# Performance work log

Measured on AMD Instinct MI355X. Metric: run time of the kernel, lower is better.

Reference implementation:

```python
import jax, jax.numpy as jnp
import numpy as np

R, TR = 47, 2  # response_size, treat_size


def _lstm_cell(x, h, c, Wih, Whh, bih, bhh):
    # PyTorch gate order: i, f, g, o
    gates = x @ Wih.T + h @ Whh.T + bih + bhh
    i, f, g, o = jnp.split(gates, 4, axis=-1)
    c_new = jax.nn.sigmoid(f) * c + jax.nn.sigmoid(i) * jnp.tanh(g)
    h_new = jax.nn.sigmoid(o) * jnp.tanh(c_new)
    return h_new, c_new


def setup_inputs() -> dict:
    key = jax.random.key(0)
    B, T = 256, 2048
    ks = jax.random.split(key, 20)

    def u(k, shape, H):
        s = 1.0 / np.sqrt(H).astype(np.float32)
        return jax.random.uniform(k, shape, jnp.float32, -s, s)

    return {
        "x_r": jax.random.normal(ks[0], (B, T, R), jnp.float32),
        "x_t": jax.random.normal(ks[1], (B, T, TR), jnp.float32),
        # r_rnn: 2-layer LSTM, input 49 -> hidden 47
        "r_Wih0": u(ks[2], (4 * R, R + TR), R), "r_Whh0": u(ks[3], (4 * R, R), R),
        "r_bih0": u(ks[4], (4 * R,), R), "r_bhh0": u(ks[5], (4 * R,), R),
        "r_Wih1": u(ks[6], (4 * R, R), R), "r_Whh1": u(ks[7], (4 * R, R), R),
        "r_bih1": u(ks[8], (4 * R,), R), "r_bhh1": u(ks[9], (4 * R,), R),
        # t_rnn: 2-layer LSTM, input 96 -> hidden 2
        "t_Wih0": u(ks[10], (4 * TR, 2 * R + TR), TR), "t_Whh0": u(ks[11], (4 * TR, TR), TR),
        "t_bih0": u(ks[12], (4 * TR,), TR), "t_bhh0": u(ks[13], (4 * TR,), TR),
        "t_Wih1": u(ks[14], (4 * TR, TR), TR), "t_Whh1": u(ks[15], (4 * TR, TR), TR),
        "t_bih1": u(ks[16], (4 * TR,), TR), "t_bhh1": u(ks[17], (4 * TR,), TR),
    }


def reference(x_r, x_t,
              r_Wih0, r_Whh0, r_bih0, r_bhh0, r_Wih1, r_Whh1, r_bih1, r_bhh1,
              t_Wih0, t_Whh0, t_bih0, t_bhh0, t_Wih1, t_Whh1, t_bih1, t_bhh1):
    B = x_r.shape[0]
    zR = jnp.zeros((B, R), x_r.dtype)
    zT = jnp.zeros((B, TR), x_r.dtype)

    def step(carry, xs):
        hr0, cr0, hr1, cr1, ht0, ct0, ht1, ct1 = carry
        r, t = xs  # [B,47], [B,2]
        r_in = jnp.concatenate([r, t], axis=-1)              # [B,49]
        hr0, cr0 = _lstm_cell(r_in, hr0, cr0, r_Wih0, r_Whh0, r_bih0, r_bhh0)
        hr1, cr1 = _lstm_cell(hr0, hr1, cr1, r_Wih1, r_Whh1, r_bih1, r_bhh1)
        t_in = jnp.concatenate([r_in, hr1], axis=-1)         # [B,96]
        ht0, ct0 = _lstm_cell(t_in, ht0, ct0, t_Wih0, t_Whh0, t_bih0, t_bhh0)
        ht1, ct1 = _lstm_cell(ht0, ht1, ct1, t_Wih1, t_Whh1, t_bih1, t_bhh1)
        return (hr0, cr0, hr1, cr1, ht0, ct0, ht1, ct1), (hr1, ht1)

    init = (zR, zR, zR, zR, zT, zT, zT, zT)
    xs = (x_r.transpose(1, 0, 2), x_t.transpose(1, 0, 2))    # time-major
    _, (r_seq, t_seq) = jax.lax.scan(step, init, xs)         # [T,B,47], [T,B,2]
    return (r_seq.transpose(1, 0, 2), t_seq.transpose(1, 0, 2))
```

## Files before the change

### kernel.cpp

```cpp
#include <hip/hip_runtime.h>

#define T_STEPS 2048
#define TOTAL   2080

typedef float f2 __attribute__((ext_vector_type(2)));
typedef _Float16 h2 __attribute__((ext_vector_type(2)));

__device__ __forceinline__ float fast_rcp(float x) { return __builtin_amdgcn_rcpf(x); }

__device__ __forceinline__ float sig_f(float x) {
    return fast_rcp(1.0f + __expf(-x));
}
__device__ __forceinline__ float tanh_f(float x) {
    float e = __expf(-2.0f * x);
    return fmaf(2.0f, fast_rcp(1.0f + e), -1.0f);
}
__device__ __forceinline__ float gate_act(float x, float zm, float sm, float sa) {
    float e = __expf(-x * zm);
    return fmaf(fast_rcp(1.0f + e), sm, sa);
}

#if __has_builtin(__builtin_amdgcn_fdot2)
#define FDOT2(a, b, c) __builtin_amdgcn_fdot2((a), (b), (c), false)
#else
__device__ __forceinline__ float FDOT2(h2 a, h2 b, float c) {
    return fmaf((float)a.x, (float)b.x, fmaf((float)a.y, (float)b.y, c));
}
#endif

#define LDS_BARRIER() asm volatile("s_waitcnt lgkmcnt(0)\n\ts_barrier" ::: "memory")

#define DPP_BCAST0 0x00
#define DPP_BCAST1 0x55
#define DPP_BCAST2 0xAA
#define DPP_BCAST3 0xFF
#define DPP_PAIR   0xF5
#define DPP_ROR4   0x124
#define DPP_ROR8   0x128
template<int CTRL>
__device__ __forceinline__ float dppf(float x) {
    int r = __builtin_amdgcn_update_dpp(0, __builtin_bit_cast(int, x), CTRL, 0xF, 0xF, true);
    return __builtin_bit_cast(float, r);
}

__device__ __forceinline__ void loadx4(float (&dst)[4], const float* __restrict__ x_r,
                                       const float* __restrict__ x_t,
                                       size_t xrb, size_t xtb, int l) {
#pragma unroll
    for (int u = 0; u < 4; ++u) {
        int v = l + 16 * u;
        dst[u] = (v < 47) ? x_r[xrb + v] : ((v < 49) ? x_t[xtb + (v - 47)] : 0.0f);
    }
}

__device__ __forceinline__ void unpack12(f2 (&in)[24], const float4* __restrict__ r4) {
#pragma unroll
    for (int u = 0; u < 12; ++u) {
        float4 v = r4[u];
        in[2 * u]     = f2{v.x, v.y};
        in[2 * u + 1] = f2{v.z, v.w};
    }
}

__device__ __forceinline__ void unpackh(h2 (&in)[24], const h2* __restrict__ row) {
    const float4* q = (const float4*)row;
#pragma unroll
    for (int k = 0; k < 6; ++k) {
        float4 v = q[k];
        in[4 * k + 0] = __builtin_bit_cast(h2, v.x);
        in[4 * k + 1] = __builtin_bit_cast(h2, v.y);
        in[4 * k + 2] = __builtin_bit_cast(h2, v.z);
        in[4 * k + 3] = __builtin_bit_cast(h2, v.w);
    }
}

__device__ __forceinline__ float4 dot4h(const h2 (&in)[24], const h2 (&w)[4][24], float4 init) {
    float a0 = init.x, a1 = init.y, a2 = init.z, a3 = init.w;
#pragma unroll
    for (int u = 0; u < 24; ++u) {
        a0 = FDOT2(w[0][u], in[u], a0);
        a1 = FDOT2(w[1][u], in[u], a1);
        a2 = FDOT2(w[2][u], in[u], a2);
        a3 = FDOT2(w[3][u], in[u], a3);
    }
    return float4{a0, a1, a2, a3};
}

__device__ __forceinline__ void loadw47h(h2 (&w)[24], const float* __restrict__ src) {
#pragma unroll
    for (int u = 0; u < 23; ++u)
        w[u] = h2{(_Float16)src[2 * u], (_Float16)src[2 * u + 1]};
    w[23] = h2{(_Float16)src[46], (_Float16)0.0f};
}

__global__ __launch_bounds__(320) void adrnn_fused(
    const float* __restrict__ x_r, const float* __restrict__ x_t,
    const float* __restrict__ rWih0, const float* __restrict__ rWhh0,
    const float* __restrict__ rbih0, const float* __restrict__ rbhh0,
    const float* __restrict__ rWih1, const float* __restrict__ rWhh1,
    const float* __restrict__ rbih1, const float* __restrict__ rbhh1,
    const float* __restrict__ tWih0, const float* __restrict__ tWhh0,
    const float* __restrict__ tbih0, const float* __restrict__ tbhh0,
    const float* __restrict__ tWih1, const float* __restrict__ tWhh1,
    const float* __restrict__ tbih1, const float* __restrict__ tbhh1,
    float* __restrict__ r_out, float* __restrict__ t_out)
{
    __shared__ __align__(16) float tring[64][112];
    __shared__ __align__(16) h2 h0f16[16][32];
    __shared__ __align__(16) h2 h1f16[16][32];
    __shared__ __align__(16) float pAring[16][192];
    __shared__ __align__(16) float pBring[16][192];

    const int tid = threadIdx.x;
    const int wid = tid >> 6;
    const int l   = tid & 63;
    const int j   = l;
    const int b = blockIdx.x;
    const size_t xr_base = (size_t)b * T_STEPS * 47;
    const size_t xt_base = (size_t)b * T_STEPS * 2;

    if (tid < 256) {
        for (int k = tid; k < 64 * 48; k += 256) tring[k / 48][64 + (k % 48)] = 0.0f;
        for (int k = tid; k < 16 * 32; k += 256) {
            h0f16[k >> 5][k & 31] = h2{(_Float16)0.0f, (_Float16)0.0f};
            h1f16[k >> 5][k & 31] = h2{(_Float16)0.0f, (_Float16)0.0f};
        }
    }

    if (wid == 0) {
        f2 w[4][24]; float w48[4]; float4 bias = {0, 0, 0, 0};
#pragma unroll
        for (int g = 0; g < 4; ++g) { w48[g] = 0.f;
#pragma unroll
            for (int u = 0; u < 24; ++u) w[g][u] = f2{0.f, 0.f}; }
        if (j < 47) {
            float bb[4];
#pragma unroll
            for (int g = 0; g < 4; ++g) {
                const int row = g * 47 + j;
#pragma unroll
                for (int u = 0; u < 24; ++u)
                    w[g][u] = f2{rWih0[row * 49 + 2 * u], rWih0[row * 49 + 2 * u + 1]};
                w48[g] = rWih0[row * 49 + 48];
                bb[g] = rbih0[row] + rbhh0[row];
            }
            bias = {bb[0], bb[1], bb[2], bb[3]};
        }
        const int jsw4 = (j ^ (j >> 3)) * 4;
        __syncthreads();
        for (int i = 0; i < TOTAL; ++i) {
            if (i < T_STEPS && j < 47) {
                f2 in[24];
                unpack12(in, (const float4*)&tring[i & 63][0]);
                float x48 = tring[i & 63][48];
                f2 a0 = f2{bias.x, 0.f}, a1 = f2{bias.y, 0.f}, a2 = f2{bias.z, 0.f}, a3 = f2{bias.w, 0.f};
#pragma unroll
                for (int u = 0; u < 24; ++u) {
                    a0 = __builtin_elementwise_fma(w[0][u], in[u], a0);
                    a1 = __builtin_elementwise_fma(w[1][u], in[u], a1);
                    a2 = __builtin_elementwise_fma(w[2][u], in[u], a2);
                    a3 = __builtin_elementwise_fma(w[3][u], in[u], a3);
                }
                float4 out;
                out.x = fmaf(w48[0], x48, a0.x + a0.y);
                out.y = fmaf(w48[1], x48, a1.x + a1.y);
                out.z = fmaf(w48[2], x48, a2.x + a2.y);
                out.w = fmaf(w48[3], x48, a3.x + a3.y);
                *(float4*)&pAring[i & 15][jsw4] = out;
            }
            if ((i & 7) == 7) LDS_BARRIER();
        }
    } else if (wid == 1) {
        h2 w[4][24];
#pragma unroll
        for (int g = 0; g < 4; ++g)
#pragma unroll
            for (int u = 0; u < 24; ++u) w[g][u] = h2{(_Float16)0.0f, (_Float16)0.0f};
        if (j < 47) {
#pragma unroll
            for (int g = 0; g < 4; ++g) loadw47h(w[g], &rWhh0[(g * 47 + j) * 47]);
        }
        const int jsw4 = (j ^ (j >> 3)) * 4;
        float c0 = 0.f;
        __syncthreads();
        for (int i = 0; i < TOTAL; ++i) {
            const int s = i - 8;
            float hv = 0.0f;
            if (s >= 0 && s < T_STEPS && j < 47) {
                float4 pa = *(const float4*)&pAring[s & 15][jsw4];
                h2 in[24];
                unpackh(in, &h0f16[(s - 1) & 15][0]);
                float4 pre = dot4h(in, w, pa);
                float iv = sig_f(pre.x), fv = sig_f(pre.y);
                float gv = tanh_f(pre.z), ov = sig_f(pre.w);
                c0 = fmaf(fv, c0, iv * gv);
                hv = ov * tanh_f(c0);
            }
            float hn = dppf<DPP_PAIR>(hv);
            if (s >= 0 && s < T_STEPS && j < 47 && !(j & 1)) {
                h0f16[s & 15][j >> 1] = __builtin_bit_cast(h2, __builtin_amdgcn_cvt_pkrtz(hv, hn));
            }
            if ((i & 7) == 7) LDS_BARRIER();
        }
    } else if (wid == 2) {
        h2 w[4][24]; float4 bias = {0, 0, 0, 0};
#pragma unroll
        for (int g = 0; g < 4; ++g)
#pragma unroll
            for (int u = 0; u < 24; ++u) w[g][u] = h2{(_Float16)0.0f, (_Float16)0.0f};
        if (j < 47) {
            float bb[4];
#pragma unroll
            for (int g = 0; g < 4; ++g) {
                loadw47h(w[g], &rWih1[(g * 47 + j) * 47]);
                bb[g] = rbih1[g * 47 + j] + rbhh1[g * 47 + j];
            }
            bias = {bb[0], bb[1], bb[2], bb[3]};
        }
        const int jsw4 = (j ^ (j >> 3)) * 4;
        __syncthreads();
        for (int i = 0; i < TOTAL; ++i) {
            const int s = i - 16;
            if (s >= 0 && s < T_STEPS && j < 47) {
                h2 in[24];
                unpackh(in, &h0f16[s & 15][0]);
                float4 pre = dot4h(in, w, bias);
                *(float4*)&pBring[s & 15][jsw4] = pre;
            }
            if ((i & 7) == 7) LDS_BARRIER();
        }
    } else if (wid == 3) {
        h2 w[4][24];
#pragma unroll
        for (int g = 0; g < 4; ++g)
#pragma unroll
            for (int u = 0; u < 24; ++u) w[g][u] = h2{(_Float16)0.0f, (_Float16)0.0f};
        if (j < 47) {
#pragma unroll
            for (int g = 0; g < 4; ++g) loadw47h(w[g], &rWhh1[(g * 47 + j) * 47]);
        }
        const int jsw4 = (j ^ (j >> 3)) * 4;
        float c1 = 0.f;
        __syncthreads();
        for (int i = 0; i < TOTAL; ++i) {
            const int s = i - 24;
            float hv = 0.0f;
            if (s >= 0 && s < T_STEPS && j < 47) {
                float4 pb = *(const float4*)&pBring[s & 15][jsw4];
                h2 in[24];
                unpackh(in, &h1f16[(s - 1) & 15][0]);
                float4 pre = dot4h(in, w, pb);
                float iv = sig_f(pre.x), fv = sig_f(pre.y);
                float gv = tanh_f(pre.z), ov = sig_f(pre.w);
                c1 = fmaf(fv, c1, iv * gv);
                hv = ov * tanh_f(c1);
                tring[s & 63][64 + j] = hv;
                r_out[((size_t)b * T_STEPS + s) * 47 + j] = hv;
            }
            float hn = dppf<DPP_PAIR>(hv);
            if (s >= 0 && s < T_STEPS && j < 47 && !(j & 1)) {
                h1f16[s & 15][j >> 1] = __builtin_bit_cast(h2, __builtin_amdgcn_cvt_pkrtz(hv, hn));
            }
            if ((i & 7) == 7) LDS_BARRIER();
        }
    } else {
        const int u  = (l >> 2) & 1;
        const int g  = l & 3;
        const int hf = (l >> 3) & 1;
        const int R0 = g * 2 + u;
        f2 wt[24]; float wx48;
        if (hf == 0) {
            wx48 = 0.f;
#pragma unroll
            for (int k = 0; k < 24; ++k)
                wt[k] = f2{tWih0[R0 * 96 + 2 * k], tWih0[R0 * 96 + 2 * k + 1]};
        } else {
            wx48 = tWih0[R0 * 96 + 48];
#pragma unroll
            for (int k = 0; k < 23; ++k)
                wt[k] = f2{tWih0[R0 * 96 + 49 + 2 * k], tWih0[R0 * 96 + 49 + 2 * k + 1]};
            wt[23] = f2{tWih0[R0 * 96 + 95], 0.f};
        }
        const float bT0 = tbih0[R0] + tbhh0[R0];
        const float wh00 = tWhh0[R0 * 2 + 0], wh01 = tWhh0[R0 * 2 + 1];
        const float wi10 = tWih1[R0 * 2 + 0], wi11 = tWih1[R0 * 2 + 1];
        const float wh10 = tWhh1[R0 * 2 + 0], wh11 = tWhh1[R0 * 2 + 1];
        const float bT1 = tbih1[R0] + tbhh1[R0];
        const bool isg = (g == 2);
        const float zm = isg ? 2.f : 1.f, sm = isg ? 2.f : 1.f, sa = isg ? -1.f : 0.f;
        float ht00 = 0.f, ht01 = 0.f, ct0u = 0.f;
        float ht10 = 0.f, ht11 = 0.f, ct1u = 0.f;

        float xa[4] = {0,0,0,0}, xb[4] = {0,0,0,0}, xc[4] = {0,0,0,0};
        if (l < 16) {
            for (int t = 0; t < 8; ++t) {
                float xv[4];
                loadx4(xv, x_r, x_t, xr_base + (size_t)t * 47, xt_base + (size_t)t * 2, l);
#pragma unroll
                for (int uu = 0; uu < 4; ++uu) {
                    int v = l + 16 * uu;
                    if (v < 49) tring[t][v] = xv[uu];
                }
            }
            loadx4(xa, x_r, x_t, xr_base + (size_t)8 * 47,  xt_base + (size_t)8 * 2,  l);
            loadx4(xb, x_r, x_t, xr_base + (size_t)9 * 47,  xt_base + (size_t)9 * 2,  l);
            loadx4(xc, x_r, x_t, xr_base + (size_t)10 * 47, xt_base + (size_t)10 * 2, l);
        }
        __syncthreads();

        for (int i = 0; i < TOTAL; ++i) {
            if (l < 16) {
                const int tw = i + 8;
                if (tw < T_STEPS) {
#pragma unroll
                    for (int uu = 0; uu < 4; ++uu) {
                        int v = l + 16 * uu;
                        if (v < 49) tring[tw & 63][v] = xa[uu];
                    }
                }
#pragma unroll
                for (int uu = 0; uu < 4; ++uu) { xa[uu] = xb[uu]; xb[uu] = xc[uu]; }
                int tl = i + 11;
                if (tl > T_STEPS - 1) tl = T_STEPS - 1;
                loadx4(xc, x_r, x_t, xr_base + (size_t)tl * 47, xt_base + (size_t)tl * 2, l);
            }
            const int s = i - 32;
            if (s >= 0 && s < T_STEPS) {
                f2 in[24];
                unpack12(in, (const float4*)&tring[s & 63][hf ? 64 : 0]);
                float x48 = tring[s & 63][48];
                f2 av = {0, 0}, bv = {0, 0};
#pragma unroll
                for (int k = 0; k < 12; ++k) {
                    av = __builtin_elementwise_fma(wt[2 * k],     in[2 * k],     av);
                    bv = __builtin_elementwise_fma(wt[2 * k + 1], in[2 * k + 1], bv);
                }
                f2 sv = av + bv;
                float part = fmaf(wx48, x48, sv.x + sv.y);
                float pre0 = part + dppf<DPP_ROR8>(part);
                pre0 += bT0 + wh00 * ht00 + wh01 * ht01;
                float a0 = gate_act(pre0, zm, sm, sa);
                float i0 = dppf<DPP_BCAST0>(a0);
                float f0 = dppf<DPP_BCAST1>(a0);
                float g0 = dppf<DPP_BCAST2>(a0);
                float o0 = dppf<DPP_BCAST3>(a0);
                ct0u = fmaf(f0, ct0u, i0 * g0);
                float htu = o0 * tanh_f(ct0u);
                float hto = dppf<DPP_ROR4>(htu);
                ht00 = (u == 0) ? htu : hto;
                ht01 = (u == 0) ? hto : htu;
                float pre1 = bT1 + wi10 * ht00 + wi11 * ht01 + wh10 * ht10 + wh11 * ht11;
                float a1 = gate_act(pre1, zm, sm, sa);
                float ji = dppf<DPP_BCAST0>(a1);
                float jf = dppf<DPP_BCAST1>(a1);
                float jg = dppf<DPP_BCAST2>(a1);
                float jo = dppf<DPP_BCAST3>(a1);
                ct1u = fmaf(jf, ct1u, ji * jg);
                float h1u = jo * tanh_f(ct1u);
                float h1o = dppf<DPP_ROR4>(h1u);
                ht10 = (u == 0) ? h1u : h1o;
                ht11 = (u == 0) ? h1o : h1u;
                if (l == 0) {
                    float2 tv = {ht10, ht11};
                    *reinterpret_cast<float2*>(&t_out[((size_t)b * T_STEPS + s) * 2]) = tv;
                }
            }
            if ((i & 7) == 7) LDS_BARRIER();
        }
    }
}

extern "C" void kernel_launch(void* const* d_in, const int* in_sizes, int n_in,
                              void* d_out, int out_size, void* d_ws, size_t ws_size,
                              hipStream_t stream) {
    const float* x_r   = (const float*)d_in[0];
    const float* x_t   = (const float*)d_in[1];
    const float* rWih0 = (const float*)d_in[2];
    const float* rWhh0 = (const float*)d_in[3];
    const float* rbih0 = (const float*)d_in[4];
    const float* rbhh0 = (const float*)d_in[5];
    const float* rWih1 = (const float*)d_in[6];
    const float* rWhh1 = (const float*)d_in[7];
    const float* rbih1 = (const float*)d_in[8];
    const float* rbhh1 = (const float*)d_in[9];
    const float* tWih0 = (const float*)d_in[10];
    const float* tWhh0 = (const float*)d_in[11];
    const float* tbih0 = (const float*)d_in[12];
    const float* tbhh0 = (const float*)d_in[13];
    const float* tWih1 = (const float*)d_in[14];
    const float* tWhh1 = (const float*)d_in[15];
    const float* tbih1 = (const float*)d_in[16];
    const float* tbhh1 = (const float*)d_in[17];

    float* r_out = (float*)d_out;
    float* t_out = r_out + (size_t)256 * T_STEPS * 47;

    hipLaunchKernelGGL(adrnn_fused, dim3(256), dim3(320), 0, stream,
                       x_r, x_t, rWih0, rWhh0, rbih0, rbhh0, rWih1, rWhh1, rbih1, rbhh1,
                       tWih0, tWhh0, tbih0, tbhh0, tWih1, tWhh1, tbih1, tbhh1,
                       r_out, t_out);
}
```

Baseline: 1.445 ms.

## Merge wavefront roles to run four waves per block instead of five

Reassigns the pipelined LSTM stages from five wavefronts to four. The x-prefetch ring loader moves into wave 0 alongside the layer-0 input projection, and the layer-1 input projection is merged with the t_rnn wave. The block shrinks from 320 to 256 threads, which cuts barrier participants and per-block wave count. It also splits the wave-0 FMA chains into two accumulators for more ILP and drops the XOR swizzle on the pA/pB ring indices. The risk is that the merged waves now carry more serial work per step, which may lengthen the critical path, and the unswizzled rings may cause LDS bank conflicts.

```diff
diff --git a/kernel.cpp b/kernel.cpp
--- a/kernel.cpp
+++ b/kernel.cpp
@@ -8,9 +8,7 @@
 
 __device__ __forceinline__ float fast_rcp(float x) { return __builtin_amdgcn_rcpf(x); }
 
-__device__ __forceinline__ float sig_f(float x) {
-    return fast_rcp(1.0f + __expf(-x));
-}
+__device__ __forceinline__ float sig_f(float x) { return fast_rcp(1.0f + __expf(-x)); }
 __device__ __forceinline__ float tanh_f(float x) {
     float e = __expf(-2.0f * x);
     return fmaf(2.0f, fast_rcp(1.0f + e), -1.0f);
@@ -93,7 +91,7 @@
     w[23] = h2{(_Float16)src[46], (_Float16)0.0f};
 }
 
-__global__ __launch_bounds__(320) void adrnn_fused(
+__global__ __launch_bounds__(256) void adrnn_fused(
     const float* __restrict__ x_r, const float* __restrict__ x_t,
     const float* __restrict__ rWih0, const float* __restrict__ rWhh0,
     const float* __restrict__ rbih0, const float* __restrict__ rbhh0,
@@ -119,7 +117,7 @@
     const size_t xr_base = (size_t)b * T_STEPS * 47;
     const size_t xt_base = (size_t)b * T_STEPS * 2;
 
-    if (tid < 256) {
+    {
         for (int k = tid; k < 64 * 48; k += 256) tring[k / 48][64 + (k % 48)] = 0.0f;
         for (int k = tid; k < 16 * 32; k += 256) {
             h0f16[k >> 5][k & 31] = h2{(_Float16)0.0f, (_Float16)0.0f};
@@ -146,27 +144,64 @@
             }
             bias = {bb[0], bb[1], bb[2], bb[3]};
         }
-        const int jsw4 = (j ^ (j >> 3)) * 4;
+        float xa[4] = {0,0,0,0}, xb[4] = {0,0,0,0}, xc[4] = {0,0,0,0};
+        if (l < 16) {
+            for (int t = 0; t < 8; ++t) {
+                float xv[4];
+                loadx4(xv, x_r, x_t, xr_base + (size_t)t * 47, xt_base + (size_t)t * 2, l);
+#pragma unroll
+                for (int uu = 0; uu < 4; ++uu) {
+                    int v = l + 16 * uu;
+                    if (v < 49) tring[t][v] = xv[uu];
+                }
+            }
+            loadx4(xa, x_r, x_t, xr_base + (size_t)8 * 47,  xt_base + (size_t)8 * 2,  l);
+            loadx4(xb, x_r, x_t, xr_base + (size_t)9 * 47,  xt_base + (size_t)9 * 2,  l);
+            loadx4(xc, x_r, x_t, xr_base + (size_t)10 * 47, xt_base + (size_t)10 * 2, l);
+        }
         __syncthreads();
         for (int i = 0; i < TOTAL; ++i) {
             if (i < T_STEPS && j < 47) {
                 f2 in[24];
                 unpack12(in, (const float4*)&tring[i & 63][0]);
                 float x48 = tring[i & 63][48];
-                f2 a0 = f2{bias.x, 0.f}, a1 = f2{bias.y, 0.f}, a2 = f2{bias.z, 0.f}, a3 = f2{bias.w, 0.f};
-#pragma unroll
-                for (int u = 0; u < 24; ++u) {
-                    a0 = __builtin_elementwise_fma(w[0][u], in[u], a0);
-                    a1 = __builtin_elementwise_fma(w[1][u], in[u], a1);
-                    a2 = __builtin_elementwise_fma(w[2][u], in[u], a2);
-                    a3 = __builtin_elementwise_fma(w[3][u], in[u], a3);
-                }
+                f2 a0 = f2{bias.x, 0.f}, b0v = {0, 0};
+                f2 a1 = f2{bias.y, 0.f}, b1v = {0, 0};
+                f2 a2 = f2{bias.z, 0.f}, b2v = {0, 0};
+                f2 a3 = f2{bias.w, 0.f}, b3v = {0, 0};
+#pragma unroll
+                for (int u = 0; u < 12; ++u) {
+                    a0  = __builtin_elementwise_fma(w[0][u],      in[u],      a0);
+                    b0v = __builtin_elementwise_fma(w[0][12 + u], in[12 + u], b0v);
+                    a1  = __builtin_elementwise_fma(w[1][u],      in[u],      a1);
+                    b1v = __builtin_elementwise_fma(w[1][12 + u], in[12 + u], b1v);
+                    a2  = __builtin_elementwise_fma(w[2][u],      in[u],      a2);
+                    b2v = __builtin_elementwise_fma(w[2][12 + u], in[12 + u], b2v);
+                    a3  = __builtin_elementwise_fma(w[3][u],      in[u],      a3);
+                    b3v = __builtin_elementwise_fma(w[3][12 + u], in[12 + u], b3v);
+                }
+                f2 s0 = a0 + b0v, s1 = a1 + b1v, s2 = a2 + b2v, s3 = a3 + b3v;
                 float4 out;
-                out.x = fmaf(w48[0], x48, a0.x + a0.y);
-                out.y = fmaf(w48[1], x48, a1.x + a1.y);
-                out.z = fmaf(w48[2], x48, a2.x + a2.y);
-                out.w = fmaf(w48[3], x48, a3.x + a3.y);
-                *(float4*)&pAring[i & 15][jsw4] = out;
+                out.x = fmaf(w48[0], x48, s0.x + s0.y);
+                out.y = fmaf(w48[1], x48, s1.x + s1.y);
+                out.z = fmaf(w48[2], x48, s2.x + s2.y);
+                out.w = fmaf(w48[3], x48, s3.x + s3.y);
+                *(float4*)&pAring[i & 15][j * 4] = out;
+            }
+            if (l < 16) {
+                const int tw = i + 8;
+                if (tw < T_STEPS) {
+#pragma unroll
+                    for (int uu = 0; uu < 4; ++uu) {
+                        int v = l + 16 * uu;
+                        if (v < 49) tring[tw & 63][v] = xa[uu];
+                    }
+                }
+#pragma unroll
+                for (int uu = 0; uu < 4; ++uu) { xa[uu] = xb[uu]; xb[uu] = xc[uu]; }
+                int tl = i + 11;
+                if (tl > T_STEPS - 1) tl = T_STEPS - 1;
+                loadx4(xc, x_r, x_t, xr_base + (size_t)tl * 47, xt_base + (size_t)tl * 2, l);
             }
             if ((i & 7) == 7) LDS_BARRIER();
         }
@@ -180,14 +215,13 @@
 #pragma unroll
             for (int g = 0; g < 4; ++g) loadw47h(w[g], &rWhh0[(g * 47 + j) * 47]);
         }
-        const int jsw4 = (j ^ (j >> 3)) * 4;
         float c0 = 0.f;
         __syncthreads();
         for (int i = 0; i < TOTAL; ++i) {
             const int s = i - 8;
             float hv = 0.0f;
             if (s >= 0 && s < T_STEPS && j < 47) {
-                float4 pa = *(const float4*)&pAring[s & 15][jsw4];
+                float4 pa = *(const float4*)&pAring[s & 15][j * 4];
                 h2 in[24];
                 unpackh(in, &h0f16[(s - 1) & 15][0]);
                 float4 pre = dot4h(in, w, pa);
@@ -217,59 +251,12 @@
             }
             bias = {bb[0], bb[1], bb[2], bb[3]};
         }
-        const int jsw4 = (j ^ (j >> 3)) * 4;
-        __syncthreads();
-        for (int i = 0; i < TOTAL; ++i) {
-            const int s = i - 16;
-            if (s >= 0 && s < T_STEPS && j < 47) {
-                h2 in[24];
-                unpackh(in, &h0f16[s & 15][0]);
-                float4 pre = dot4h(in, w, bias);
-                *(float4*)&pBring[s & 15][jsw4] = pre;
-            }
-            if ((i & 7) == 7) LDS_BARRIER();
-        }
-    } else if (wid == 3) {
-        h2 w[4][24];
-#pragma unroll
-        for (int g = 0; g < 4; ++g)
-#pragma unroll
-            for (int u = 0; u < 24; ++u) w[g][u] = h2{(_Float16)0.0f, (_Float16)0.0f};
-        if (j < 47) {
-#pragma unroll
-            for (int g = 0; g < 4; ++g) loadw47h(w[g], &rWhh1[(g * 47 + j) * 47]);
-        }
-        const int jsw4 = (j ^ (j >> 3)) * 4;
-        float c1 = 0.f;
-        __syncthreads();
-        for (int i = 0; i < TOTAL; ++i) {
-            const int s = i - 24;
-            float hv = 0.0f;
-            if (s >= 0 && s < T_STEPS && j < 47) {
-                float4 pb = *(const float4*)&pBring[s & 15][jsw4];
-                h2 in[24];
-                unpackh(in, &h1f16[(s - 1) & 15][0]);
-                float4 pre = dot4h(in, w, pb);
-                float iv = sig_f(pre.x), fv = sig_f(pre.y);
-                float gv = tanh_f(pre.z), ov = sig_f(pre.w);
-                c1 = fmaf(fv, c1, iv * gv);
-                hv = ov * tanh_f(c1);
-                tring[s & 63][64 + j] = hv;
-                r_out[((size_t)b * T_STEPS + s) * 47 + j] = hv;
-            }
-            float hn = dppf<DPP_PAIR>(hv);
-            if (s >= 0 && s < T_STEPS && j < 47 && !(j & 1)) {
-                h1f16[s & 15][j >> 1] = __builtin_bit_cast(h2, __builtin_amdgcn_cvt_pkrtz(hv, hn));
-            }
-            if ((i & 7) == 7) LDS_BARRIER();
-        }
-    } else {
-        const int u  = (l >> 2) & 1;
-        const int g  = l & 3;
-        const int hf = (l >> 3) & 1;
-        const int R0 = g * 2 + u;
+        const int tu  = (l >> 2) & 1;
+        const int tg  = l & 3;
+        const int thf = (l >> 3) & 1;
+        const int R0 = tg * 2 + tu;
         f2 wt[24]; float wx48;
-        if (hf == 0) {
+        if (thf == 0) {
             wx48 = 0.f;
 #pragma unroll
             for (int k = 0; k < 24; ++k)
@@ -286,48 +273,24 @@
         const float wi10 = tWih1[R0 * 2 + 0], wi11 = tWih1[R0 * 2 + 1];
         const float wh10 = tWhh1[R0 * 2 + 0], wh11 = tWhh1[R0 * 2 + 1];
         const float bT1 = tbih1[R0] + tbhh1[R0];
-        const bool isg = (g == 2);
+        const bool isg = (tg == 2);
         const float zm = isg ? 2.f : 1.f, sm = isg ? 2.f : 1.f, sa = isg ? -1.f : 0.f;
         float ht00 = 0.f, ht01 = 0.f, ct0u = 0.f;
         float ht10 = 0.f, ht11 = 0.f, ct1u = 0.f;
 
-        float xa[4] = {0,0,0,0}, xb[4] = {0,0,0,0}, xc[4] = {0,0,0,0};
-        if (l < 16) {
-            for (int t = 0; t < 8; ++t) {
-                float xv[4];
-                loadx4(xv, x_r, x_t, xr_base + (size_t)t * 47, xt_base + (size_t)t * 2, l);
-#pragma unroll
-                for (int uu = 0; uu < 4; ++uu) {
-                    int v = l + 16 * uu;
-                    if (v < 49) tring[t][v] = xv[uu];
-                }
-            }
-            loadx4(xa, x_r, x_t, xr_base + (size_t)8 * 47,  xt_base + (size_t)8 * 2,  l);
-            loadx4(xb, x_r, x_t, xr_base + (size_t)9 * 47,  xt_base + (size_t)9 * 2,  l);
-            loadx4(xc, x_r, x_t, xr_base + (size_t)10 * 47, xt_base + (size_t)10 * 2, l);
-        }
         __syncthreads();
-
         for (int i = 0; i < TOTAL; ++i) {
-            if (l < 16) {
-                const int tw = i + 8;
-                if (tw < T_STEPS) {
-#pragma unroll
-                    for (int uu = 0; uu < 4; ++uu) {
-                        int v = l + 16 * uu;
-                        if (v < 49) tring[tw & 63][v] = xa[uu];
-                    }
-                }
-#pragma unroll
-                for (int uu = 0; uu < 4; ++uu) { xa[uu] = xb[uu]; xb[uu] = xc[uu]; }
-                int tl = i + 11;
-                if (tl > T_STEPS - 1) tl = T_STEPS - 1;
-                loadx4(xc, x_r, x_t, xr_base + (size_t)tl * 47, xt_base + (size_t)tl * 2, l);
+            const int s2 = i - 16;
+            if (s2 >= 0 && s2 < T_STEPS && j < 47) {
+                h2 in[24];
+                unpackh(in, &h0f16[s2 & 15][0]);
+                float4 pre = dot4h(in, w, bias);
+                *(float4*)&pBring[s2 & 15][j * 4] = pre;
             }
             const int s = i - 32;
             if (s >= 0 && s < T_STEPS) {
                 f2 in[24];
-                unpack12(in, (const float4*)&tring[s & 63][hf ? 64 : 0]);
+                unpack12(in, (const float4*)&tring[s & 63][thf ? 64 : 0]);
                 float x48 = tring[s & 63][48];
                 f2 av = {0, 0}, bv = {0, 0};
 #pragma unroll
@@ -347,8 +310,8 @@
                 ct0u = fmaf(f0, ct0u, i0 * g0);
                 float htu = o0 * tanh_f(ct0u);
                 float hto = dppf<DPP_ROR4>(htu);
-                ht00 = (u == 0) ? htu : hto;
-                ht01 = (u == 0) ? hto : htu;
+                ht00 = (tu == 0) ? htu : hto;
+                ht01 = (tu == 0) ? hto : htu;
                 float pre1 = bT1 + wi10 * ht00 + wi11 * ht01 + wh10 * ht10 + wh11 * ht11;
                 float a1 = gate_act(pre1, zm, sm, sa);
                 float ji = dppf<DPP_BCAST0>(a1);
@@ -358,12 +321,45 @@
                 ct1u = fmaf(jf, ct1u, ji * jg);
                 float h1u = jo * tanh_f(ct1u);
                 float h1o = dppf<DPP_ROR4>(h1u);
-                ht10 = (u == 0) ? h1u : h1o;
-                ht11 = (u == 0) ? h1o : h1u;
+                ht10 = (tu == 0) ? h1u : h1o;
+                ht11 = (tu == 0) ? h1o : h1u;
                 if (l == 0) {
                     float2 tv = {ht10, ht11};
                     *reinterpret_cast<float2*>(&t_out[((size_t)b * T_STEPS + s) * 2]) = tv;
                 }
+            }
+            if ((i & 7) == 7) LDS_BARRIER();
+        }
+    } else {
+        h2 w[4][24];
+#pragma unroll
+        for (int g = 0; g < 4; ++g)
+#pragma unroll
+            for (int u = 0; u < 24; ++u) w[g][u] = h2{(_Float16)0.0f, (_Float16)0.0f};
+        if (j < 47) {
+#pragma unroll
+            for (int g = 0; g < 4; ++g) loadw47h(w[g], &rWhh1[(g * 47 + j) * 47]);
+        }
+        float c1 = 0.f;
+        __syncthreads();
+        for (int i = 0; i < TOTAL; ++i) {
+            const int s = i - 24;
+            float hv = 0.0f;
+            if (s >= 0 && s < T_STEPS && j < 47) {
+                float4 pb = *(const float4*)&pBring[s & 15][j * 4];
+                h2 in[24];
+                unpackh(in, &h1f16[(s - 1) & 15][0]);
+                float4 pre = dot4h(in, w, pb);
+                float iv = sig_f(pre.x), fv = sig_f(pre.y);
+                float gv = tanh_f(pre.z), ov = sig_f(pre.w);
+                c1 = fmaf(fv, c1, iv * gv);
+                hv = ov * tanh_f(c1);
+                tring[s & 63][64 + j] = hv;
+                r_out[((size_t)b * T_STEPS + s) * 47 + j] = hv;
+            }
+            float hn = dppf<DPP_PAIR>(hv);
+            if (s >= 0 && s < T_STEPS && j < 47 && !(j & 1)) {
+                h1f16[s & 15][j >> 1] = __builtin_bit_cast(h2, __builtin_amdgcn_cvt_pkrtz(hv, hn));
             }
             if ((i & 7) == 7) LDS_BARRIER();
         }
@@ -395,7 +391,7 @@
     float* r_out = (float*)d_out;
     float* t_out = r_out + (size_t)256 * T_STEPS * 47;
 
-    hipLaunchKernelGGL(adrnn_fused, dim3(256), dim3(320), 0, stream,
+    hipLaunchKernelGGL(adrnn_fused, dim3(256), dim3(256), 0, stream,
                        x_r, x_t, rWih0, rWhh0, rbih0, rbhh0, rWih1, rWhh1, rbih1, rbhh1,
                        tWih0, tWhh0, tbih0, tbhh0, tWih1, tWhh1, tbih1, tbhh1,
                        r_out, t_out);
```

Measured after the change: 1.452 ms. About the same (+0.5%).
